# Optimization experiments

Hardware: AMD Instinct MI355X
Metric: run time of the kernel (lower is better)

The kernel has to match this reference:

```python
import jax, jax.numpy as jnp
import numpy as np

NUM_USERS = 200000
NUM_ITEMS = 100000
NUM_NODES = NUM_USERS + NUM_ITEMS
EMBED_DIM = 64
NUM_EDGES = 2000000
NUM_LAYERS = 2


def setup_inputs() -> dict:
    key = jax.random.key(0)
    k1, k2, k3, k4, k5 = jax.random.split(key, 5)
    u_embs = jax.random.normal(k1, (NUM_USERS, EMBED_DIM), dtype=jnp.float32)
    i_embs = jax.random.normal(k2, (NUM_ITEMS, EMBED_DIM), dtype=jnp.float32)
    edge_src = jax.random.randint(k3, (NUM_EDGES,), 0, NUM_NODES, dtype=jnp.int32)
    edge_dst = jax.random.randint(k4, (NUM_EDGES,), 0, NUM_NODES, dtype=jnp.int32)
    # precomputed symmetric-normalized adjacency weights (1/sqrt(du*di) in the original)
    edge_weight = jax.random.uniform(k5, (NUM_EDGES,), dtype=jnp.float32)
    return {
        "u_embs": u_embs,
        "i_embs": i_embs,
        "edge_src": edge_src,
        "edge_dst": edge_dst,
        "edge_weight": edge_weight,
    }


def _gcn_smooth(embs, edge_src, edge_dst, edge_weight):
    # sparse SpMM: out[d] = sum_{e: dst(e)=d} w_e * embs[src(e)]
    msgs = embs[edge_src] * edge_weight[:, None]  # [E, D]
    return jax.ops.segment_sum(msgs, edge_dst, num_segments=NUM_NODES)


def reference(u_embs, i_embs, edge_src, edge_dst, edge_weight):
    all_embs = jnp.concatenate([u_embs, i_embs], axis=0)  # [N, D]
    acc = all_embs  # running sum over layer outputs (layer 0 included)
    x = all_embs
    for _ in range(NUM_LAYERS):
        x = _gcn_smooth(x, edge_src, edge_dst, edge_weight)
        acc = acc + x
    return acc / jnp.float32(NUM_LAYERS + 1)  # mean over stacked layers
```

## Files before the change

### kernel.cpp

```cpp
#include <hip/hip_runtime.h>
#include <hip/hip_bf16.h>

#define NUSERS 200000
#define NITEMS 100000
#define NNODES 300000
#define EDIM   64
#define NEDGES 2000000
#define SCAN_NB ((NNODES + 255) / 256)
#define FILL_BLOCKS 2048
#define NPASS 4

typedef unsigned short u16;

__device__ __forceinline__ float bf2f(u16 h) {
    return __uint_as_float((unsigned)h << 16);
}
__device__ __forceinline__ u16 f2bf(float f) {
    union { __hip_bfloat16 b; u16 u; } c;
    c.b = __float2bfloat16(f);
    return c.u;
}


__global__ void k_hist(const int4* __restrict__ dst4, int* __restrict__ cnt) {
    int i = blockIdx.x * 256 + threadIdx.x;
    if (i < NEDGES / 4) {
        int4 d = dst4[i];
        atomicAdd(&cnt[d.x], 1);
        atomicAdd(&cnt[d.y], 1);
        atomicAdd(&cnt[d.z], 1);
        atomicAdd(&cnt[d.w], 1);
    }
}

__global__ void k_scan1(int* __restrict__ data, int* __restrict__ bsum) {
    __shared__ int s[256];
    int i = blockIdx.x * 256 + threadIdx.x;
    int v = (i < NNODES) ? data[i] : 0;
    s[threadIdx.x] = v;
    __syncthreads();
    for (int o = 1; o < 256; o <<= 1) {
        int t = (threadIdx.x >= o) ? s[threadIdx.x - o] : 0;
        __syncthreads();
        s[threadIdx.x] += t;
        __syncthreads();
    }
    if (i < NNODES) data[i] = s[threadIdx.x] - v;
    if (threadIdx.x == 255) bsum[blockIdx.x] = s[255];
}

__global__ void k_scan2(int* __restrict__ bsum) {
    __shared__ int s[256];
    __shared__ int carry;
    if (threadIdx.x == 0) carry = 0;
    __syncthreads();
    for (int base = 0; base < SCAN_NB; base += 256) {
        int i = base + threadIdx.x;
        int v = (i < SCAN_NB) ? bsum[i] : 0;
        s[threadIdx.x] = v;
        __syncthreads();
        for (int o = 1; o < 256; o <<= 1) {
            int t = (threadIdx.x >= o) ? s[threadIdx.x - o] : 0;
            __syncthreads();
            s[threadIdx.x] += t;
            __syncthreads();
        }
        if (i < SCAN_NB) bsum[i] = s[threadIdx.x] - v + carry;
        __syncthreads();
        if (threadIdx.x == 0) carry += s[255];
        __syncthreads();
    }
}

__global__ void k_scan3(int* __restrict__ off, const int* __restrict__ bscan,
                        int* __restrict__ wpos) {
    int i = blockIdx.x * 256 + threadIdx.x;
    if (i < NNODES) {
        int v = off[i] + bscan[blockIdx.x];
        off[i] = v;
        wpos[i] = v;
    }
}

__global__ void k_fill_win(const int* __restrict__ src, const int4* __restrict__ dst4,
                           const float* __restrict__ w, int* __restrict__ wpos,
                           int2* __restrict__ edata) {
    const int W = (NNODES + NPASS - 1) / NPASS;
    for (int k = 0; k < NPASS; ++k) {
        int lo = k * W;
        int hi = lo + W;
        for (int i = blockIdx.x * 256 + threadIdx.x; i < NEDGES / 4;
             i += FILL_BLOCKS * 256) {
            int4 d = dst4[i];
            int e = i * 4;
            if (d.x >= lo && d.x < hi) {
                int p = atomicAdd(&wpos[d.x], 1);
                edata[p] = make_int2(src[e], __float_as_int(w[e]));
            }
            if (d.y >= lo && d.y < hi) {
                int p = atomicAdd(&wpos[d.y], 1);
                edata[p] = make_int2(src[e + 1], __float_as_int(w[e + 1]));
            }
            if (d.z >= lo && d.z < hi) {
                int p = atomicAdd(&wpos[d.z], 1);
                edata[p] = make_int2(src[e + 2], __float_as_int(w[e + 2]));
            }
            if (d.w >= lo && d.w < hi) {
                int p = atomicAdd(&wpos[d.w], 1);
                edata[p] = make_int2(src[e + 3], __float_as_int(w[e + 3]));
            }
        }
    }
}

__global__ void k_convert(const float4* __restrict__ uq, const float4* __restrict__ iq,
                          ushort4* __restrict__ xb4) {
    int i = blockIdx.x * 256 + threadIdx.x;
    const int uq_n = NUSERS * 16;
    const int nq_n = NNODES * 16;
    if (i >= nq_n) return;
    float4 v = (i < uq_n) ? uq[i] : iq[i - uq_n];
    ushort4 h;
    h.x = f2bf(v.x); h.y = f2bf(v.y); h.z = f2bf(v.z); h.w = f2bf(v.w);
    xb4[i] = h;
}


__device__ __forceinline__ float4 bfrow(const ushort4* __restrict__ xb4, int s, int l16) {
    ushort4 h = xb4[(size_t)s * 16 + l16];
    float4 v;
    v.x = bf2f(h.x); v.y = bf2f(h.y); v.z = bf2f(h.z); v.w = bf2f(h.w);
    return v;
}

__global__ void k_spmm1(const ushort4* __restrict__ xb4,
                        const int* __restrict__ off, const int2* __restrict__ edata,
                        ushort4* __restrict__ x1b4) {
    int node = blockIdx.x * 4 + (threadIdx.x >> 6);
    if (node >= NNODES) return;
    int lane = threadIdx.x & 63;
    int q = lane >> 4;
    int l16 = lane & 15;
    int p = off[node] + q;
    int end = (node == NNODES - 1) ? NEDGES : off[node + 1];
    float4 a0 = make_float4(0.f, 0.f, 0.f, 0.f);
    float4 a1 = make_float4(0.f, 0.f, 0.f, 0.f);
    for (; p + 4 < end; p += 8) {
        int2 e0 = edata[p];
        int2 e1 = edata[p + 4];
        float4 v0 = bfrow(xb4, e0.x, l16);
        float4 v1 = bfrow(xb4, e1.x, l16);
        float w0 = __int_as_float(e0.y), w1 = __int_as_float(e1.y);
        a0.x += w0 * v0.x; a0.y += w0 * v0.y; a0.z += w0 * v0.z; a0.w += w0 * v0.w;
        a1.x += w1 * v1.x; a1.y += w1 * v1.y; a1.z += w1 * v1.z; a1.w += w1 * v1.w;
    }
    if (p < end) {
        int2 e0 = edata[p];
        float4 v0 = bfrow(xb4, e0.x, l16);
        float w0 = __int_as_float(e0.y);
        a0.x += w0 * v0.x; a0.y += w0 * v0.y; a0.z += w0 * v0.z; a0.w += w0 * v0.w;
    }
    a0.x += a1.x; a0.y += a1.y; a0.z += a1.z; a0.w += a1.w;
    a0.x += __shfl_xor(a0.x, 16, 64); a0.y += __shfl_xor(a0.y, 16, 64);
    a0.z += __shfl_xor(a0.z, 16, 64); a0.w += __shfl_xor(a0.w, 16, 64);
    a0.x += __shfl_xor(a0.x, 32, 64); a0.y += __shfl_xor(a0.y, 32, 64);
    a0.z += __shfl_xor(a0.z, 32, 64); a0.w += __shfl_xor(a0.w, 32, 64);
    if (q == 0) {
        ushort4 h;
        h.x = f2bf(a0.x); h.y = f2bf(a0.y); h.z = f2bf(a0.z); h.w = f2bf(a0.w);
        x1b4[(size_t)node * 16 + l16] = h;
    }
}

__global__ void k_spmm2(const float4* __restrict__ uq, const float4* __restrict__ iq,
                        const ushort4* __restrict__ x1b4,
                        const int* __restrict__ off, const int2* __restrict__ edata,
                        float4* __restrict__ outq) {
    int node = blockIdx.x * 4 + (threadIdx.x >> 6);
    if (node >= NNODES) return;
    int lane = threadIdx.x & 63;
    int q = lane >> 4;
    int l16 = lane & 15;
    int p = off[node] + q;
    int end = (node == NNODES - 1) ? NEDGES : off[node + 1];
    float4 a0 = make_float4(0.f, 0.f, 0.f, 0.f);
    float4 a1 = make_float4(0.f, 0.f, 0.f, 0.f);
    for (; p + 4 < end; p += 8) {
        int2 e0 = edata[p];
        int2 e1 = edata[p + 4];
        float4 v0 = bfrow(x1b4, e0.x, l16);
        float4 v1 = bfrow(x1b4, e1.x, l16);
        float w0 = __int_as_float(e0.y), w1 = __int_as_float(e1.y);
        a0.x += w0 * v0.x; a0.y += w0 * v0.y; a0.z += w0 * v0.z; a0.w += w0 * v0.w;
        a1.x += w1 * v1.x; a1.y += w1 * v1.y; a1.z += w1 * v1.z; a1.w += w1 * v1.w;
    }
    if (p < end) {
        int2 e0 = edata[p];
        float4 v0 = bfrow(x1b4, e0.x, l16);
        float w0 = __int_as_float(e0.y);
        a0.x += w0 * v0.x; a0.y += w0 * v0.y; a0.z += w0 * v0.z; a0.w += w0 * v0.w;
    }
    a0.x += a1.x; a0.y += a1.y; a0.z += a1.z; a0.w += a1.w;
    a0.x += __shfl_xor(a0.x, 16, 64); a0.y += __shfl_xor(a0.y, 16, 64);
    a0.z += __shfl_xor(a0.z, 16, 64); a0.w += __shfl_xor(a0.w, 16, 64);
    a0.x += __shfl_xor(a0.x, 32, 64); a0.y += __shfl_xor(a0.y, 32, 64);
    a0.z += __shfl_xor(a0.z, 32, 64); a0.w += __shfl_xor(a0.w, 32, 64);
    if (q == 0) {
        size_t ridx = (size_t)node * 16 + l16;
        float4 x0 = (node < NUSERS) ? uq[ridx] : iq[ridx - (size_t)NUSERS * 16];
        float4 x1v = bfrow(x1b4, node, l16);
        const float s = 1.0f / 3.0f;
        float4 r;
        r.x = (x0.x + x1v.x + a0.x) * s;
        r.y = (x0.y + x1v.y + a0.y) * s;
        r.z = (x0.z + x1v.z + a0.z) * s;
        r.w = (x0.w + x1v.w + a0.w) * s;
        outq[ridx] = r;
    }
}


__global__ void scatter_l1(const float* __restrict__ u, const float* __restrict__ it,
                           float* __restrict__ y,
                           const int* __restrict__ src, const int* __restrict__ dst,
                           const float* __restrict__ w) {
    long long t = (long long)blockIdx.x * blockDim.x + threadIdx.x;
    int e = (int)(t >> 4);
    if (e >= NEDGES) return;
    int q = (int)(t & 15);
    int s = src[e], d = dst[e];
    float we = w[e];
    const float* xrow = (s < NUSERS) ? (u + (size_t)s * EDIM)
                                     : (it + (size_t)(s - NUSERS) * EDIM);
    float4 v = ((const float4*)xrow)[q];
    float* yp = y + (size_t)d * EDIM + q * 4;
    atomicAdd(yp + 0, we * v.x);
    atomicAdd(yp + 1, we * v.y);
    atomicAdd(yp + 2, we * v.z);
    atomicAdd(yp + 3, we * v.w);
}

__global__ void scatter_gen(const float* __restrict__ x, float* __restrict__ y,
                            const int* __restrict__ src, const int* __restrict__ dst,
                            const float* __restrict__ w) {
    long long t = (long long)blockIdx.x * blockDim.x + threadIdx.x;
    int e = (int)(t >> 4);
    if (e >= NEDGES) return;
    int q = (int)(t & 15);
    int s = src[e], d = dst[e];
    float we = w[e];
    float4 v = ((const float4*)(x + (size_t)s * EDIM))[q];
    float* yp = y + (size_t)d * EDIM + q * 4;
    atomicAdd(yp + 0, we * v.x);
    atomicAdd(yp + 1, we * v.y);
    atomicAdd(yp + 2, we * v.z);
    atomicAdd(yp + 3, we * v.w);
}

__global__ void final_kernel(const float4* __restrict__ u, const float4* __restrict__ it,
                             const float4* __restrict__ x2, float4* __restrict__ outq) {
    int i = blockIdx.x * blockDim.x + threadIdx.x;
    const int uq = NUSERS * EDIM / 4;
    const int nq = NNODES * EDIM / 4;
    if (i >= nq) return;
    float4 x0 = (i < uq) ? u[i] : it[i - uq];
    float4 x1 = outq[i];
    float4 a  = x2[i];
    const float s = 1.0f / 3.0f;
    float4 r;
    r.x = (x0.x + x1.x + a.x) * s;
    r.y = (x0.y + x1.y + a.y) * s;
    r.z = (x0.z + x1.z + a.z) * s;
    r.w = (x0.w + x1.w + a.w) * s;
    outq[i] = r;
}


extern "C" void kernel_launch(void* const* d_in, const int* in_sizes, int n_in,
                              void* d_out, int out_size, void* d_ws, size_t ws_size,
                              hipStream_t stream) {
    const float* u   = (const float*)d_in[0];
    const float* it  = (const float*)d_in[1];
    const int*   src = (const int*)d_in[2];
    const int*   dst = (const int*)d_in[3];
    const float* w   = (const float*)d_in[4];
    float* out = (float*)d_out;

    const size_t nd = (size_t)NNODES * EDIM;

    int*     off   = (int*)d_ws;
    int*     wpos  = off + NNODES;
    int*     bscan = wpos + NNODES;
    int2*    edata = (int2*)(bscan + 2048);
    ushort4* xb4   = (ushort4*)(edata + NEDGES);
    ushort4* x1b4  = xb4 + (size_t)NNODES * 16;
    const size_t needed =
        ((size_t)NNODES * 2 + 2048 + (size_t)NEDGES * 2 +
         (size_t)NNODES * 32 * 2) * sizeof(int) / 1 ;

    const int eb4 = (NEDGES / 4 + 255) / 256;
    const int nb4 = (NNODES + 3) / 4;
    const int cb  = (NNODES * 16 + 255) / 256;
    dim3 blk(256);

    if (ws_size >= needed) {
        hipMemsetAsync(off, 0, (size_t)NNODES * sizeof(int), stream);
        k_hist <<<eb4, blk, 0, stream>>>((const int4*)dst, off);
        k_scan1<<<SCAN_NB, blk, 0, stream>>>(off, bscan);
        k_scan2<<<1, blk, 0, stream>>>(bscan);
        k_scan3<<<SCAN_NB, blk, 0, stream>>>(off, bscan, wpos);
        k_fill_win<<<FILL_BLOCKS, blk, 0, stream>>>(src, (const int4*)dst, w, wpos, edata);
        k_convert<<<cb, blk, 0, stream>>>((const float4*)u, (const float4*)it, xb4);
        k_spmm1<<<nb4, blk, 0, stream>>>(xb4, off, edata, x1b4);
        k_spmm2<<<nb4, blk, 0, stream>>>((const float4*)u, (const float4*)it,
                                         x1b4, off, edata, (float4*)out);
    } else {
        float* A = (float*)d_ws;
        hipMemsetAsync(out, 0, nd * sizeof(float), stream);
        long long nthreads = (long long)NEDGES * 16;
        int sblocks = (int)((nthreads + 255) / 256);
        scatter_l1<<<sblocks, blk, 0, stream>>>(u, it, out, src, dst, w);
        hipMemsetAsync(A, 0, nd * sizeof(float), stream);
        scatter_gen<<<sblocks, blk, 0, stream>>>(out, A, src, dst, w);
        final_kernel<<<(NNODES * EDIM / 4 + 255) / 256, blk, 0, stream>>>(
            (const float4*)u, (const float4*)it, (const float4*)A, (float4*)out);
    }
}
```

Before: 530.2 us.

## Use persistent grid-stride SpMM with prefetched offsets and batched edge loads; fuse hist+convert

Fuses the degree histogram and the bf16 conversion into one launch. The SpMM kernels become persistent grid-stride kernels with fixed block counts, prefetch the next node's offsets, and issue four clamped edge and row loads up front to raise memory-level parallelism, with a loop for tails longer than 16 edges. A sentinel off[NNODES] removes the last-node branch, and the address math uses 32-bit shifts. Fewer, longer-lived blocks may reduce latency hiding, and low-degree nodes now pay for redundant clamped edge loads.

New measurement: 515.8 us. 2.7% less time.

```diff
diff --git a/kernel.cpp b/kernel.cpp
--- a/kernel.cpp
+++ b/kernel.cpp
@@ -9,6 +9,10 @@
 #define SCAN_NB ((NNODES + 255) / 256)
 #define FILL_BLOCKS 2048
 #define NPASS 4
+#define EB4 ((NEDGES / 4 + 255) / 256)
+#define CB  ((NNODES * 16 + 255) / 256)
+#define SPMM_BLOCKS 2048
+#define SPMM_STRIDE (SPMM_BLOCKS * 4)
 
 typedef unsigned short u16;
 
@@ -21,17 +25,30 @@
     return c.u;
 }
 
-
-__global__ void k_hist(const int4* __restrict__ dst4, int* __restrict__ cnt) {
-    int i = blockIdx.x * 256 + threadIdx.x;
-    if (i < NEDGES / 4) {
-        int4 d = dst4[i];
-        atomicAdd(&cnt[d.x], 1);
-        atomicAdd(&cnt[d.y], 1);
-        atomicAdd(&cnt[d.z], 1);
-        atomicAdd(&cnt[d.w], 1);
-    }
-}
+__global__ void k_prep(const int4* __restrict__ dst4, int* __restrict__ cnt,
+                       const float4* __restrict__ uq, const float4* __restrict__ iq,
+                       ushort4* __restrict__ xb4) {
+    int b = blockIdx.x;
+    if (b < EB4) {
+        int i = b * 256 + threadIdx.x;
+        if (i < NEDGES / 4) {
+            int4 d = dst4[i];
+            atomicAdd(&cnt[d.x], 1);
+            atomicAdd(&cnt[d.y], 1);
+            atomicAdd(&cnt[d.z], 1);
+            atomicAdd(&cnt[d.w], 1);
+        }
+    } else {
+        int i = (b - EB4) * 256 + threadIdx.x;
+        if (i < NNODES * 16) {
+            float4 v = (i < NUSERS * 16) ? uq[i] : iq[i - NUSERS * 16];
+            ushort4 h;
+            h.x = f2bf(v.x); h.y = f2bf(v.y); h.z = f2bf(v.z); h.w = f2bf(v.w);
+            xb4[i] = h;
+        }
+    }
+}
+
 
 __global__ void k_scan1(int* __restrict__ data, int* __restrict__ bsum) {
     __shared__ int s[256];
@@ -80,7 +97,9 @@
         off[i] = v;
         wpos[i] = v;
     }
-}
+    if (i == 0) off[NNODES] = NEDGES;
+}
+
 
 __global__ void k_fill_win(const int* __restrict__ src, const int4* __restrict__ dst4,
                            const float* __restrict__ w, int* __restrict__ wpos,
@@ -113,109 +132,145 @@
     }
 }
 
-__global__ void k_convert(const float4* __restrict__ uq, const float4* __restrict__ iq,
-                          ushort4* __restrict__ xb4) {
-    int i = blockIdx.x * 256 + threadIdx.x;
-    const int uq_n = NUSERS * 16;
-    const int nq_n = NNODES * 16;
-    if (i >= nq_n) return;
-    float4 v = (i < uq_n) ? uq[i] : iq[i - uq_n];
-    ushort4 h;
-    h.x = f2bf(v.x); h.y = f2bf(v.y); h.z = f2bf(v.z); h.w = f2bf(v.w);
-    xb4[i] = h;
-}
-
 
 __device__ __forceinline__ float4 bfrow(const ushort4* __restrict__ xb4, int s, int l16) {
-    ushort4 h = xb4[(size_t)s * 16 + l16];
+    const ushort4* p = (const ushort4*)((const char*)xb4 +
+                       (((unsigned)s << 7) + ((unsigned)l16 << 3)));
+    ushort4 h = *p;
     float4 v;
     v.x = bf2f(h.x); v.y = bf2f(h.y); v.z = bf2f(h.z); v.w = bf2f(h.w);
     return v;
 }
 
-__global__ void k_spmm1(const ushort4* __restrict__ xb4,
-                        const int* __restrict__ off, const int2* __restrict__ edata,
-                        ushort4* __restrict__ x1b4) {
-    int node = blockIdx.x * 4 + (threadIdx.x >> 6);
-    if (node >= NNODES) return;
-    int lane = threadIdx.x & 63;
-    int q = lane >> 4;
-    int l16 = lane & 15;
-    int p = off[node] + q;
-    int end = (node == NNODES - 1) ? NEDGES : off[node + 1];
-    float4 a0 = make_float4(0.f, 0.f, 0.f, 0.f);
-    float4 a1 = make_float4(0.f, 0.f, 0.f, 0.f);
-    for (; p + 4 < end; p += 8) {
-        int2 e0 = edata[p];
-        int2 e1 = edata[p + 4];
-        float4 v0 = bfrow(xb4, e0.x, l16);
-        float4 v1 = bfrow(xb4, e1.x, l16);
+__device__ __forceinline__ int2 ld_edge(const int2* __restrict__ e, int i) {
+    return *(const int2*)((const char*)e + ((unsigned)i << 3));
+}
+
+__global__ __launch_bounds__(256, 8)
+void k_spmm1(const ushort4* __restrict__ xb4, const int* __restrict__ off,
+             const int2* __restrict__ edata, ushort4* __restrict__ x1b4) {
+    const int wid  = threadIdx.x >> 6;
+    const int lane = threadIdx.x & 63;
+    const int q    = lane >> 4;
+    const int l16  = lane & 15;
+    int n = blockIdx.x * 4 + wid;
+    int o0 = off[n];
+    int o1 = off[n + 1];
+    while (n < NNODES) {
+        int nn = n + SPMM_STRIDE;
+        int no0 = 0, no1 = 0;
+        if (nn < NNODES) { no0 = off[nn]; no1 = off[nn + 1]; }
+        int deg = o1 - o0;
+        int cap = o1 - 1; if (cap < 0) cap = 0;
+        int b0 = o0 + q;
+        int p0 = b0;      if (p0 > cap) p0 = cap;
+        int p1 = b0 + 4;  if (p1 > cap) p1 = cap;
+        int p2 = b0 + 8;  if (p2 > cap) p2 = cap;
+        int p3 = b0 + 12; if (p3 > cap) p3 = cap;
+        int2 e0 = ld_edge(edata, p0);
+        int2 e1 = ld_edge(edata, p1);
+        int2 e2 = ld_edge(edata, p2);
+        int2 e3 = ld_edge(edata, p3);
+        float4 v0 = make_float4(0.f, 0.f, 0.f, 0.f);
+        float4 v1 = v0, v2 = v0, v3 = v0;
+        if (q < deg)      v0 = bfrow(xb4, e0.x, l16);
+        if (q + 4 < deg)  v1 = bfrow(xb4, e1.x, l16);
+        if (q + 8 < deg)  v2 = bfrow(xb4, e2.x, l16);
+        if (q + 12 < deg) v3 = bfrow(xb4, e3.x, l16);
         float w0 = __int_as_float(e0.y), w1 = __int_as_float(e1.y);
-        a0.x += w0 * v0.x; a0.y += w0 * v0.y; a0.z += w0 * v0.z; a0.w += w0 * v0.w;
-        a1.x += w1 * v1.x; a1.y += w1 * v1.y; a1.z += w1 * v1.z; a1.w += w1 * v1.w;
-    }
-    if (p < end) {
-        int2 e0 = edata[p];
-        float4 v0 = bfrow(xb4, e0.x, l16);
-        float w0 = __int_as_float(e0.y);
-        a0.x += w0 * v0.x; a0.y += w0 * v0.y; a0.z += w0 * v0.z; a0.w += w0 * v0.w;
-    }
-    a0.x += a1.x; a0.y += a1.y; a0.z += a1.z; a0.w += a1.w;
-    a0.x += __shfl_xor(a0.x, 16, 64); a0.y += __shfl_xor(a0.y, 16, 64);
-    a0.z += __shfl_xor(a0.z, 16, 64); a0.w += __shfl_xor(a0.w, 16, 64);
-    a0.x += __shfl_xor(a0.x, 32, 64); a0.y += __shfl_xor(a0.y, 32, 64);
-    a0.z += __shfl_xor(a0.z, 32, 64); a0.w += __shfl_xor(a0.w, 32, 64);
-    if (q == 0) {
-        ushort4 h;
-        h.x = f2bf(a0.x); h.y = f2bf(a0.y); h.z = f2bf(a0.z); h.w = f2bf(a0.w);
-        x1b4[(size_t)node * 16 + l16] = h;
-    }
-}
-
-__global__ void k_spmm2(const float4* __restrict__ uq, const float4* __restrict__ iq,
-                        const ushort4* __restrict__ x1b4,
-                        const int* __restrict__ off, const int2* __restrict__ edata,
-                        float4* __restrict__ outq) {
-    int node = blockIdx.x * 4 + (threadIdx.x >> 6);
-    if (node >= NNODES) return;
-    int lane = threadIdx.x & 63;
-    int q = lane >> 4;
-    int l16 = lane & 15;
-    int p = off[node] + q;
-    int end = (node == NNODES - 1) ? NEDGES : off[node + 1];
-    float4 a0 = make_float4(0.f, 0.f, 0.f, 0.f);
-    float4 a1 = make_float4(0.f, 0.f, 0.f, 0.f);
-    for (; p + 4 < end; p += 8) {
-        int2 e0 = edata[p];
-        int2 e1 = edata[p + 4];
-        float4 v0 = bfrow(x1b4, e0.x, l16);
-        float4 v1 = bfrow(x1b4, e1.x, l16);
+        float w2 = __int_as_float(e2.y), w3 = __int_as_float(e3.y);
+        float4 a0, a1;
+        a0.x = w0 * v0.x; a0.y = w0 * v0.y; a0.z = w0 * v0.z; a0.w = w0 * v0.w;
+        a1.x = w1 * v1.x; a1.y = w1 * v1.y; a1.z = w1 * v1.z; a1.w = w1 * v1.w;
+        a0.x += w2 * v2.x; a0.y += w2 * v2.y; a0.z += w2 * v2.z; a0.w += w2 * v2.w;
+        a1.x += w3 * v3.x; a1.y += w3 * v3.y; a1.z += w3 * v3.z; a1.w += w3 * v3.w;
+        if (deg > 16) {
+            for (int p = b0 + 16; p < o1; p += 4) {
+                int2 e = ld_edge(edata, p);
+                float4 v = bfrow(xb4, e.x, l16);
+                float w = __int_as_float(e.y);
+                a0.x += w * v.x; a0.y += w * v.y; a0.z += w * v.z; a0.w += w * v.w;
+            }
+        }
+        a0.x += a1.x; a0.y += a1.y; a0.z += a1.z; a0.w += a1.w;
+        a0.x += __shfl_xor(a0.x, 16, 64); a0.y += __shfl_xor(a0.y, 16, 64);
+        a0.z += __shfl_xor(a0.z, 16, 64); a0.w += __shfl_xor(a0.w, 16, 64);
+        a0.x += __shfl_xor(a0.x, 32, 64); a0.y += __shfl_xor(a0.y, 32, 64);
+        a0.z += __shfl_xor(a0.z, 32, 64); a0.w += __shfl_xor(a0.w, 32, 64);
+        if (q == 0) {
+            ushort4 h;
+            h.x = f2bf(a0.x); h.y = f2bf(a0.y); h.z = f2bf(a0.z); h.w = f2bf(a0.w);
+            x1b4[(size_t)n * 16 + l16] = h;
+        }
+        n = nn; o0 = no0; o1 = no1;
+    }
+}
+
+__global__ __launch_bounds__(256, 8)
+void k_spmm2(const float4* __restrict__ uq, const float4* __restrict__ iq,
+             const ushort4* __restrict__ x1b4, const int* __restrict__ off,
+             const int2* __restrict__ edata, float4* __restrict__ outq) {
+    const int wid  = threadIdx.x >> 6;
+    const int lane = threadIdx.x & 63;
+    const int q    = lane >> 4;
+    const int l16  = lane & 15;
+    int n = blockIdx.x * 4 + wid;
+    int o0 = off[n];
+    int o1 = off[n + 1];
+    while (n < NNODES) {
+        int nn = n + SPMM_STRIDE;
+        int no0 = 0, no1 = 0;
+        if (nn < NNODES) { no0 = off[nn]; no1 = off[nn + 1]; }
+        int deg = o1 - o0;
+        int cap = o1 - 1; if (cap < 0) cap = 0;
+        int b0 = o0 + q;
+        int p0 = b0;      if (p0 > cap) p0 = cap;
+        int p1 = b0 + 4;  if (p1 > cap) p1 = cap;
+        int p2 = b0 + 8;  if (p2 > cap) p2 = cap;
+        int p3 = b0 + 12; if (p3 > cap) p3 = cap;
+        int2 e0 = ld_edge(edata, p0);
+        int2 e1 = ld_edge(edata, p1);
+        int2 e2 = ld_edge(edata, p2);
+        int2 e3 = ld_edge(edata, p3);
+        float4 v0 = make_float4(0.f, 0.f, 0.f, 0.f);
+        float4 v1 = v0, v2 = v0, v3 = v0;
+        if (q < deg)      v0 = bfrow(x1b4, e0.x, l16);
+        if (q + 4 < deg)  v1 = bfrow(x1b4, e1.x, l16);
+        if (q + 8 < deg)  v2 = bfrow(x1b4, e2.x, l16);
+        if (q + 12 < deg) v3 = bfrow(x1b4, e3.x, l16);
         float w0 = __int_as_float(e0.y), w1 = __int_as_float(e1.y);
-        a0.x += w0 * v0.x; a0.y += w0 * v0.y; a0.z += w0 * v0.z; a0.w += w0 * v0.w;
-        a1.x += w1 * v1.x; a1.y += w1 * v1.y; a1.z += w1 * v1.z; a1.w += w1 * v1.w;
-    }
-    if (p < end) {
-        int2 e0 = edata[p];
-        float4 v0 = bfrow(x1b4, e0.x, l16);
-        float w0 = __int_as_float(e0.y);
-        a0.x += w0 * v0.x; a0.y += w0 * v0.y; a0.z += w0 * v0.z; a0.w += w0 * v0.w;
-    }
-    a0.x += a1.x; a0.y += a1.y; a0.z += a1.z; a0.w += a1.w;
-    a0.x += __shfl_xor(a0.x, 16, 64); a0.y += __shfl_xor(a0.y, 16, 64);
-    a0.z += __shfl_xor(a0.z, 16, 64); a0.w += __shfl_xor(a0.w, 16, 64);
-    a0.x += __shfl_xor(a0.x, 32, 64); a0.y += __shfl_xor(a0.y, 32, 64);
-    a0.z += __shfl_xor(a0.z, 32, 64); a0.w += __shfl_xor(a0.w, 32, 64);
-    if (q == 0) {
-        size_t ridx = (size_t)node * 16 + l16;
-        float4 x0 = (node < NUSERS) ? uq[ridx] : iq[ridx - (size_t)NUSERS * 16];
-        float4 x1v = bfrow(x1b4, node, l16);
-        const float s = 1.0f / 3.0f;
-        float4 r;
-        r.x = (x0.x + x1v.x + a0.x) * s;
-        r.y = (x0.y + x1v.y + a0.y) * s;
-        r.z = (x0.z + x1v.z + a0.z) * s;
-        r.w = (x0.w + x1v.w + a0.w) * s;
-        outq[ridx] = r;
+        float w2 = __int_as_float(e2.y), w3 = __int_as_float(e3.y);
+        float4 a0, a1;
+        a0.x = w0 * v0.x; a0.y = w0 * v0.y; a0.z = w0 * v0.z; a0.w = w0 * v0.w;
+        a1.x = w1 * v1.x; a1.y = w1 * v1.y; a1.z = w1 * v1.z; a1.w = w1 * v1.w;
+        a0.x += w2 * v2.x; a0.y += w2 * v2.y; a0.z += w2 * v2.z; a0.w += w2 * v2.w;
+        a1.x += w3 * v3.x; a1.y += w3 * v3.y; a1.z += w3 * v3.z; a1.w += w3 * v3.w;
+        if (deg > 16) {
+            for (int p = b0 + 16; p < o1; p += 4) {
+                int2 e = ld_edge(edata, p);
+                float4 v = bfrow(x1b4, e.x, l16);
+                float w = __int_as_float(e.y);
+                a0.x += w * v.x; a0.y += w * v.y; a0.z += w * v.z; a0.w += w * v.w;
+            }
+        }
+        a0.x += a1.x; a0.y += a1.y; a0.z += a1.z; a0.w += a1.w;
+        a0.x += __shfl_xor(a0.x, 16, 64); a0.y += __shfl_xor(a0.y, 16, 64);
+        a0.z += __shfl_xor(a0.z, 16, 64); a0.w += __shfl_xor(a0.w, 16, 64);
+        a0.x += __shfl_xor(a0.x, 32, 64); a0.y += __shfl_xor(a0.y, 32, 64);
+        a0.z += __shfl_xor(a0.z, 32, 64); a0.w += __shfl_xor(a0.w, 32, 64);
+        if (q == 0) {
+            size_t ridx = (size_t)n * 16 + l16;
+            float4 x0 = (n < NUSERS) ? uq[ridx] : iq[ridx - (size_t)NUSERS * 16];
+            float4 x1v = bfrow(x1b4, n, l16);
+            const float s = 1.0f / 3.0f;
+            float4 r;
+            r.x = (x0.x + x1v.x + a0.x) * s;
+            r.y = (x0.y + x1v.y + a0.y) * s;
+            r.z = (x0.z + x1v.z + a0.z) * s;
+            r.w = (x0.w + x1v.w + a0.w) * s;
+            outq[ridx] = r;
+        }
+        n = nn; o0 = no0; o1 = no1;
     }
 }
 
@@ -289,31 +344,29 @@
     const size_t nd = (size_t)NNODES * EDIM;
 
     int*     off   = (int*)d_ws;
-    int*     wpos  = off + NNODES;
+    int*     wpos  = off + NNODES + 8;
     int*     bscan = wpos + NNODES;
     int2*    edata = (int2*)(bscan + 2048);
     ushort4* xb4   = (ushort4*)(edata + NEDGES);
     ushort4* x1b4  = xb4 + (size_t)NNODES * 16;
     const size_t needed =
-        ((size_t)NNODES * 2 + 2048 + (size_t)NEDGES * 2 +
-         (size_t)NNODES * 32 * 2) * sizeof(int) / 1 ;
-
-    const int eb4 = (NEDGES / 4 + 255) / 256;
-    const int nb4 = (NNODES + 3) / 4;
-    const int cb  = (NNODES * 16 + 255) / 256;
+        (size_t)(NNODES + 8 + NNODES + 2048) * sizeof(int) +
+        (size_t)NEDGES * sizeof(int2) +
+        (size_t)NNODES * 16 * sizeof(ushort4) * 2;
+
     dim3 blk(256);
 
     if (ws_size >= needed) {
         hipMemsetAsync(off, 0, (size_t)NNODES * sizeof(int), stream);
-        k_hist <<<eb4, blk, 0, stream>>>((const int4*)dst, off);
+        k_prep <<<EB4 + CB, blk, 0, stream>>>((const int4*)dst, off,
+                                              (const float4*)u, (const float4*)it, xb4);
         k_scan1<<<SCAN_NB, blk, 0, stream>>>(off, bscan);
         k_scan2<<<1, blk, 0, stream>>>(bscan);
         k_scan3<<<SCAN_NB, blk, 0, stream>>>(off, bscan, wpos);
         k_fill_win<<<FILL_BLOCKS, blk, 0, stream>>>(src, (const int4*)dst, w, wpos, edata);
-        k_convert<<<cb, blk, 0, stream>>>((const float4*)u, (const float4*)it, xb4);
-        k_spmm1<<<nb4, blk, 0, stream>>>(xb4, off, edata, x1b4);
-        k_spmm2<<<nb4, blk, 0, stream>>>((const float4*)u, (const float4*)it,
-                                         x1b4, off, edata, (float4*)out);
+        k_spmm1<<<SPMM_BLOCKS, blk, 0, stream>>>(xb4, off, edata, x1b4);
+        k_spmm2<<<SPMM_BLOCKS, blk, 0, stream>>>((const float4*)u, (const float4*)it,
+                                                 x1b4, off, edata, (float4*)out);
     } else {
         float* A = (float*)d_ws;
         hipMemsetAsync(out, 0, nd * sizeof(float), stream);
```
